# Optimization experiments

Hardware: AMD Instinct MI355X
Metric: run time of the kernel (lower is better)

## Reference

```python
import jax, jax.numpy as jnp
import numpy as np


def _knn_graph(x, k):
    """Faithful port of DynamicLstmGnn.knn_to_graph + get_u_v, returning the
    dense symmetrized edge-weight matrix [N, N] (the original re-sparsifies
    this same matrix via coalesce; nonzero extraction is data-dependent and
    not jit-able, so the dense matrix is the canonical output)."""
    N = x.shape[0]
    # negative squared euclidean distance: -||xi||^2 + 2 xi.xj - ||xj||^2
    xx = jnp.sum(x * x, axis=1, keepdims=True)          # [N, 1]
    inner = -2.0 * (x @ x.T)                              # [N, N]
    pairwise_distance = -xx - inner - xx.T                # [N, N], <= 0
    vals, idx = jax.lax.top_k(pairwise_distance, k)       # [N, k] largest (= closest)
    rows = jnp.repeat(jnp.arange(N), k)                   # idx_prime.flatten()
    # sparse COO -> to_dense (duplicate indices sum, matching torch.sparse)
    edges = jnp.zeros((N, N), dtype=x.dtype).at[rows, idx.ravel()].add(vals.ravel())
    edges_int = (edges > 0).astype(x.dtype)
    reflected_int = edges_int + edges_int.T
    reflected_edges = edges + edges.T
    denom = jnp.where(reflected_int == 0, jnp.ones((), x.dtype), reflected_int)
    edges = reflected_edges / denom
    diag = jnp.arange(N)
    edges = edges.at[diag, diag].set(0.0)                 # fill_diagonal_(0)
    return edges


def setup_inputs() -> dict:
    key = jax.random.key(0)
    x = jax.random.normal(key, (10000, 64), dtype=jnp.float32)
    return {"x": x, "k": 5}


def reference(x, k):
    return _knn_graph(x, k)
```

## Files before the change

### kernel.cpp

```cpp
#include <hip/hip_runtime.h>
#include <math.h>
#include <limits.h>

#define D 64
#define K 5
#define LK 8
#define GK 12
#define NSPLIT 16
#define NTILES 625
#define ROWBLK 157
#define NCOMP (ROWBLK * NSPLIT)
typedef unsigned int u32;
typedef unsigned long long u64;
typedef __bf16 bf16x8 __attribute__((ext_vector_type(8)));
typedef float  f32x4v __attribute__((ext_vector_type(4)));

__device__ __forceinline__ u32 med3u(u32 a, u32 b, u32 c) {
    u32 r;
    asm("v_med3_u32 %0, %1, %2, %3" : "=v"(r) : "v"(a), "v"(b), "v"(c));
    return r;
}

__device__ __forceinline__ u32 pack32(float v, int idx) {
    u32 u = __float_as_uint(v);
    u ^= ((u32)((int)u >> 31)) | 0x80000000u;
    return (u & 0xFFFFC000u) | ((~(u32)idx) & 0x3FFFu);
}
__device__ __forceinline__ int idx32(u32 key) { return (int)((~key) & 0x3FFFu); }

__device__ __forceinline__ u64 packKV(float v, int idx) {
    u32 u = __float_as_uint(v);
    u ^= ((u32)((int)u >> 31)) | 0x80000000u;
    return ((u64)u << 32) | (u32)(~idx);
}
__device__ __forceinline__ float unpackV(u64 key) {
    u32 hu = (u32)(key >> 32);
    return (hu & 0x80000000u) ? __uint_as_float(hu & 0x7fffffffu)
                              : __uint_as_float(~hu);
}

template<int LO, int LA, int LB, typename T>
__device__ __forceinline__ void mergeKeep(T a[LA], const T b[LB]) {
    T A[LA], B[LB], out[LO];
#pragma unroll
    for (int i = 0; i < LA; ++i) A[i] = a[i];
#pragma unroll
    for (int i = 0; i < LB; ++i) B[i] = b[i];
#pragma unroll
    for (int m = 0; m < LO; ++m) {
        bool ta = A[0] >= B[0];
        out[m] = ta ? A[0] : B[0];
#pragma unroll
        for (int i = 0; i < LA - 1; ++i) A[i] = ta ? A[i + 1] : A[i];
        A[LA - 1] = ta ? (T)0 : A[LA - 1];
#pragma unroll
        for (int i = 0; i < LB - 1; ++i) B[i] = ta ? B[i] : B[i + 1];
        B[LB - 1] = ta ? B[LB - 1] : (T)0;
    }
#pragma unroll
    for (int m = 0; m < LO; ++m) a[m] = out[m];
}

__global__ __launch_bounds__(256) void prep(
    const float* __restrict__ x, __bf16* __restrict__ xbA, float* __restrict__ xxf, int N)
{
    int g = blockIdx.x * 256 + threadIdx.x;
    const int REPACK = NTILES * 2 * 64;
    if (g < REPACK) {
        int tile = g >> 7;
        int rem  = g & 127;
        int kh   = rem >> 6;
        int lane = rem & 63;
        int q = lane >> 4, r = lane & 15;
        int row = tile * 16 + r;
        int k0  = kh * 32 + q * 8;
        const float4* p = (const float4*)(x + (size_t)row * D + k0);
        float4 v0 = p[0], v1 = p[1];
        bf16x8 o;
        o[0] = (__bf16)v0.x; o[1] = (__bf16)v0.y; o[2] = (__bf16)v0.z; o[3] = (__bf16)v0.w;
        o[4] = (__bf16)v1.x; o[5] = (__bf16)v1.y; o[6] = (__bf16)v1.z; o[7] = (__bf16)v1.w;
        ((bf16x8*)xbA)[g] = o;
        return;
    }
    int i = g - REPACK;
    if (i >= N) return;
    const float4* p = (const float4*)(x + (size_t)i * D);
    float s = 0.f;
#pragma unroll
    for (int t = 0; t < 16; ++t) {
        float4 v = p[t];
        s += v.x * v.x + v.y * v.y + v.z * v.z + v.w * v.w;
    }
    xxf[i] = s;
}

__global__ __launch_bounds__(256) void topk_zero_mfma(
    const __bf16* __restrict__ xbA, const float* __restrict__ xxf, int N,
    u32* __restrict__ wsK, float* __restrict__ outZ, long long totalF4,
    int nZero, int f4PerZ)
{
    const int bx  = blockIdx.x;
    const int tid = threadIdx.x;

    if (bx % 6 == 0) {
        int zid = bx / 6;
        if (zid >= nZero) return;
        long long s = (long long)zid * f4PerZ;
        long long e = s + f4PerZ; if (e > totalF4) e = totalF4;
        const f32x4v z = {0.f, 0.f, 0.f, 0.f};
        for (long long i = s + tid; i < e; i += 256)
            __builtin_nontemporal_store(z, (f32x4v*)(outZ + 4 * i));
        return;
    }

    const int cid = bx - (bx / 6 + 1);
    if (cid >= NCOMP) return;
    const int split = cid / ROWBLK;
    const int rb    = cid - split * ROWBLK;

    const int lane = tid & 63;
    const int wave = tid >> 6;
    const int l15  = lane & 15;
    const int q    = lane >> 4;
    const int r0 = rb * 64 + wave * 16;

    const bf16x8* fb = (const bf16x8*)xbA;

    int bt = r0 >> 4; if (bt > NTILES - 1) bt = NTILES - 1;
    const bf16x8 B0 = fb[bt * 128 + lane];
    const bf16x8 B1 = fb[bt * 128 + 64 + lane];

    const bf16x8* ap = fb + (size_t)split * 128 + lane;
    const float* xcp = xxf + split * 16 + q * 4;
    int cbase = split * 16 + q * 4;
    const int apBump = NSPLIT * 128;
    const int xcBump = NSPLIT * 16;

    u32 L[LK];
#pragma unroll
    for (int m = 0; m < LK; ++m) L[m] = 0u;

    for (int t = split; t < NTILES; t += NSPLIT) {
        const bf16x8 A0 = ap[0];
        const bf16x8 A1 = ap[64];
        const f32x4v xc = *(const f32x4v*)xcp;
        ap += apBump;
        xcp += xcBump;

        f32x4v acc = {0.f, 0.f, 0.f, 0.f};
        acc = __builtin_amdgcn_mfma_f32_16x16x32_bf16(A0, B0, acc, 0, 0, 0);
        acc = __builtin_amdgcn_mfma_f32_16x16x32_bf16(A1, B1, acc, 0, 0, 0);

#pragma unroll
        for (int v = 0; v < 4; ++v) {
            float dk = fmaf(-0.5f, xc[v], acc[v]);
            u32 key = pack32(dk, cbase + v);
            u32 n0 = max(L[0], key);
            u32 n1 = med3u(L[0], L[1], key);
            u32 n2 = med3u(L[1], L[2], key);
            u32 n3 = med3u(L[2], L[3], key);
            u32 n4 = med3u(L[3], L[4], key);
            u32 n5 = med3u(L[4], L[5], key);
            u32 n6 = med3u(L[5], L[6], key);
            u32 n7 = med3u(L[6], L[7], key);
            L[0]=n0; L[1]=n1; L[2]=n2; L[3]=n3; L[4]=n4; L[5]=n5; L[6]=n6; L[7]=n7;
        }
        cbase += xcBump;
    }

#pragma unroll
    for (int mask = 16; mask <= 32; mask <<= 1) {
        u32 P[LK];
#pragma unroll
        for (int m = 0; m < LK; ++m) P[m] = (u32)__shfl_xor((int)L[m], mask);
        mergeKeep<LK, LK, LK, u32>(L, P);
    }

    if (lane < 16) {
        int row = r0 + l15;
        if (row < N) {
            u32* dst = wsK + ((size_t)row * NSPLIT + split) * LK;
#pragma unroll
            for (int m = 0; m < LK; ++m) dst[m] = L[m];
        }
    }
}

__global__ __launch_bounds__(256) void rescore_scatter(
    const u32* __restrict__ wsK, const float* __restrict__ x, const float* __restrict__ xxf,
    float* __restrict__ out, int N)
{
    const int lane = threadIdx.x & 63;
    const int wave = threadIdx.x >> 6;
    const int sub  = lane & 3;
    const int row  = blockIdx.x * 64 + wave * 16 + (lane >> 2);
    const bool vrow = (row < N);
    const int rr = vrow ? row : 0;

    u32 cur[GK];
    {
        const u32* Lp = wsK + ((size_t)rr * NSPLIT + 4 * sub) * LK;
#pragma unroll
        for (int m = 0; m < LK; ++m) cur[m] = Lp[m];
#pragma unroll
        for (int m = LK; m < GK; ++m) cur[m] = 0u;
#pragma unroll
        for (int l = 1; l < 4; ++l) {
            u32 b[LK];
#pragma unroll
            for (int m = 0; m < LK; ++m) b[m] = Lp[l * LK + m];
            mergeKeep<GK, GK, LK, u32>(cur, b);
        }
    }
#pragma unroll
    for (int mask = 1; mask <= 2; mask <<= 1) {
        u32 P[GK];
#pragma unroll
        for (int m = 0; m < GK; ++m) P[m] = (u32)__shfl_xor((int)cur[m], mask);
        mergeKeep<GK, GK, GK, u32>(cur, P);
    }

    const float nxi = xxf[rr];
    int   cj[3]; bool cval[3];
    float d[3] = {0.f, 0.f, 0.f};
    const f32x4v* pj[3];
#pragma unroll
    for (int c = 0; c < 3; ++c) {
        int j = idx32(cur[sub * 3 + c]);
        cval[c] = (j < N) && (cur[sub * 3 + c] != 0u);
        cj[c] = cval[c] ? j : 0;
        pj[c] = (const f32x4v*)(x + (size_t)cj[c] * D);
    }
    const f32x4v* xip = (const f32x4v*)(x + (size_t)rr * D);
#pragma unroll
    for (int t = 0; t < 16; ++t) {
        const f32x4v xv = xip[t];
#pragma unroll
        for (int c = 0; c < 3; ++c) {
            const f32x4v pv = pj[c][t];
            d[c] = fmaf(xv[0], pv[0], d[c]);
            d[c] = fmaf(xv[1], pv[1], d[c]);
            d[c] = fmaf(xv[2], pv[2], d[c]);
            d[c] = fmaf(xv[3], pv[3], d[c]);
        }
    }
    u64 F[K];
#pragma unroll
    for (int c = 0; c < 3; ++c) {
        float val = 2.f * d[c] - nxi - xxf[cj[c]];
        F[c] = cval[c] ? packKV(val, cj[c]) : 0ull;
    }
    F[3] = 0ull; F[4] = 0ull;
    { u64 a0=F[0],a1=F[1],a2=F[2];
      if (a0 < a1) { u64 t0=a0; a0=a1; a1=t0; }
      if (a1 < a2) { u64 t0=a1; a1=a2; a2=t0; }
      if (a0 < a1) { u64 t0=a0; a0=a1; a1=t0; }
      F[0]=a0; F[1]=a1; F[2]=a2; }
#pragma unroll
    for (int mask = 1; mask <= 2; mask <<= 1) {
        u64 P[K];
#pragma unroll
        for (int m = 0; m < K; ++m) P[m] = __shfl_xor(F[m], mask);
        mergeKeep<K, K, K, u64>(F, P);
    }

    if (sub == 0 && vrow) {
#pragma unroll
        for (int m = 0; m < K; ++m) {
            int j = (int)(~(u32)F[m]);
            if ((unsigned)j < (unsigned)N && j != row) {
                float v = unpackV(F[m]);
                atomicAdd(out + (size_t)row * N + j, v);
                atomicAdd(out + (size_t)j * N + row, v);
            }
        }
    }
}

extern "C" void kernel_launch(void* const* d_in, const int* in_sizes, int n_in,
                              void* d_out, int out_size, void* d_ws, size_t ws_size,
                              hipStream_t stream) {
    const float* x = (const float*)d_in[0];
    const int N = in_sizes[0] / D;
    float* out = (float*)d_out;

    const size_t oXB = 0;
    const size_t oXX = ((size_t)NTILES * 2 * 64 * 8 * 2 + 255) & ~255ull;
    const size_t oWK = (oXX + (size_t)N * 4 + 255) & ~255ull;
    __bf16* xbA = (__bf16*)((char*)d_ws + oXB);
    float*  xxf = (float*)((char*)d_ws + oXX);
    u32*    wsK = (u32*)((char*)d_ws + oWK);

    const int prepThreads = NTILES * 2 * 64 + N;
    prep<<<(prepThreads + 255) / 256, 256, 0, stream>>>(x, xbA, xxf, N);

    long long totalF4 = (long long)out_size / 4;
    const int nBlocksTotal = 3024;
    const int nZero = (nBlocksTotal + 5) / 6;
    int f4PerZ = (int)((totalF4 + nZero - 1) / nZero);
    topk_zero_mfma<<<nBlocksTotal, 256, 0, stream>>>(
        xbA, xxf, N, wsK, out, totalF4, nZero, f4PerZ);

    rescore_scatter<<<ROWBLK, 256, 0, stream>>>(wsK, x, xxf, out, N);
}
```

Baseline: 450.7 us.

## Fuse top-k selection and rescoring into one per-tile kernel, move zeroing to prep

Merges the split top-k MFMA kernel and the rescore/scatter kernel into one kernel. Each block owns one 16-row tile, and its four waves stride over the column tiles. Partial candidate lists are merged through shared memory instead of a global workspace, and the loop prefetches the next A tile and norms. Output zeroing moves into the prep kernel, which removes one launch and the workspace round trip. In exchange, zeroing no longer overlaps the distance computation, each wave's serial selection chain is four times longer, and far fewer waves are in flight to hide latency.

```diff
diff --git a/kernel.cpp b/kernel.cpp
--- a/kernel.cpp
+++ b/kernel.cpp
@@ -1,15 +1,12 @@
 #include <hip/hip_runtime.h>
-#include <math.h>
-#include <limits.h>
 
 #define D 64
 #define K 5
 #define LK 8
 #define GK 12
-#define NSPLIT 16
 #define NTILES 625
-#define ROWBLK 157
-#define NCOMP (ROWBLK * NSPLIT)
+#define PREPBLK 352
+#define NZBLK 4096
 typedef unsigned int u32;
 typedef unsigned long long u64;
 typedef __bf16 bf16x8 __attribute__((ext_vector_type(8)));
@@ -61,91 +58,85 @@
     for (int m = 0; m < LO; ++m) a[m] = out[m];
 }
 
-__global__ __launch_bounds__(256) void prep(
-    const float* __restrict__ x, __bf16* __restrict__ xbA, float* __restrict__ xxf, int N)
+__global__ __launch_bounds__(256) void prep_zero(
+    const float* __restrict__ x, __bf16* __restrict__ xbA, float* __restrict__ xxf,
+    int N, float* __restrict__ outZ, long long totalF4, int f4PerZ)
 {
-    int g = blockIdx.x * 256 + threadIdx.x;
-    const int REPACK = NTILES * 2 * 64;
-    if (g < REPACK) {
-        int tile = g >> 7;
-        int rem  = g & 127;
-        int kh   = rem >> 6;
-        int lane = rem & 63;
-        int q = lane >> 4, r = lane & 15;
-        int row = tile * 16 + r;
-        int k0  = kh * 32 + q * 8;
-        const float4* p = (const float4*)(x + (size_t)row * D + k0);
-        float4 v0 = p[0], v1 = p[1];
-        bf16x8 o;
-        o[0] = (__bf16)v0.x; o[1] = (__bf16)v0.y; o[2] = (__bf16)v0.z; o[3] = (__bf16)v0.w;
-        o[4] = (__bf16)v1.x; o[5] = (__bf16)v1.y; o[6] = (__bf16)v1.z; o[7] = (__bf16)v1.w;
-        ((bf16x8*)xbA)[g] = o;
+    const int bx = blockIdx.x;
+    const int tid = threadIdx.x;
+
+    if (bx < PREPBLK) {
+        int g = bx * 256 + tid;
+        const int REPACK = NTILES * 2 * 64;
+        if (g < REPACK) {
+            int tile = g >> 7;
+            int rem  = g & 127;
+            int kh   = rem >> 6;
+            int lane = rem & 63;
+            int q = lane >> 4, r = lane & 15;
+            int row = tile * 16 + r;
+            int k0  = kh * 32 + q * 8;
+            const float4* p = (const float4*)(x + (size_t)row * D + k0);
+            float4 v0 = p[0], v1 = p[1];
+            bf16x8 o;
+            o[0] = (__bf16)v0.x; o[1] = (__bf16)v0.y; o[2] = (__bf16)v0.z; o[3] = (__bf16)v0.w;
+            o[4] = (__bf16)v1.x; o[5] = (__bf16)v1.y; o[6] = (__bf16)v1.z; o[7] = (__bf16)v1.w;
+            ((bf16x8*)xbA)[g] = o;
+            return;
+        }
+        int i = g - REPACK;
+        if (i >= N) return;
+        const float4* p = (const float4*)(x + (size_t)i * D);
+        float s = 0.f;
+#pragma unroll
+        for (int t = 0; t < 16; ++t) {
+            float4 v = p[t];
+            s += v.x * v.x + v.y * v.y + v.z * v.z + v.w * v.w;
+        }
+        xxf[i] = s;
         return;
     }
-    int i = g - REPACK;
-    if (i >= N) return;
-    const float4* p = (const float4*)(x + (size_t)i * D);
-    float s = 0.f;
-#pragma unroll
-    for (int t = 0; t < 16; ++t) {
-        float4 v = p[t];
-        s += v.x * v.x + v.y * v.y + v.z * v.z + v.w * v.w;
-    }
-    xxf[i] = s;
-}
-
-__global__ __launch_bounds__(256) void topk_zero_mfma(
-    const __bf16* __restrict__ xbA, const float* __restrict__ xxf, int N,
-    u32* __restrict__ wsK, float* __restrict__ outZ, long long totalF4,
-    int nZero, int f4PerZ)
+
+    int zid = bx - PREPBLK;
+    long long s = (long long)zid * f4PerZ;
+    long long e = s + f4PerZ; if (e > totalF4) e = totalF4;
+    const f32x4v z = {0.f, 0.f, 0.f, 0.f};
+    for (long long i = s + tid; i < e; i += 256)
+        __builtin_nontemporal_store(z, (f32x4v*)(outZ + 4 * i));
+}
+
+__global__ __launch_bounds__(256) void knn_select(
+    const __bf16* __restrict__ xbA, const float* __restrict__ xxf,
+    const float* __restrict__ x, int N, float* __restrict__ out)
 {
-    const int bx  = blockIdx.x;
-    const int tid = threadIdx.x;
-
-    if (bx % 6 == 0) {
-        int zid = bx / 6;
-        if (zid >= nZero) return;
-        long long s = (long long)zid * f4PerZ;
-        long long e = s + f4PerZ; if (e > totalF4) e = totalF4;
-        const f32x4v z = {0.f, 0.f, 0.f, 0.f};
-        for (long long i = s + tid; i < e; i += 256)
-            __builtin_nontemporal_store(z, (f32x4v*)(outZ + 4 * i));
-        return;
-    }
-
-    const int cid = bx - (bx / 6 + 1);
-    if (cid >= NCOMP) return;
-    const int split = cid / ROWBLK;
-    const int rb    = cid - split * ROWBLK;
-
+    const int rb   = blockIdx.x;
+    const int tid  = threadIdx.x;
     const int lane = tid & 63;
     const int wave = tid >> 6;
-    const int l15  = lane & 15;
     const int q    = lane >> 4;
-    const int r0 = rb * 64 + wave * 16;
 
     const bf16x8* fb = (const bf16x8*)xbA;
-
-    int bt = r0 >> 4; if (bt > NTILES - 1) bt = NTILES - 1;
-    const bf16x8 B0 = fb[bt * 128 + lane];
-    const bf16x8 B1 = fb[bt * 128 + 64 + lane];
-
-    const bf16x8* ap = fb + (size_t)split * 128 + lane;
-    const float* xcp = xxf + split * 16 + q * 4;
-    int cbase = split * 16 + q * 4;
-    const int apBump = NSPLIT * 128;
-    const int xcBump = NSPLIT * 16;
+    const bf16x8 B0 = fb[rb * 128 + lane];
+    const bf16x8 B1 = fb[rb * 128 + 64 + lane];
+
+    const int t0 = wave ^ 3;
+    const bf16x8* ap = fb + (size_t)t0 * 128 + lane;
+    const float*  xcp = xxf + t0 * 16 + q * 4;
+    int cbase = t0 * 16 + q * 4;
 
     u32 L[LK];
 #pragma unroll
     for (int m = 0; m < LK; ++m) L[m] = 0u;
 
-    for (int t = split; t < NTILES; t += NSPLIT) {
-        const bf16x8 A0 = ap[0];
-        const bf16x8 A1 = ap[64];
-        const f32x4v xc = *(const f32x4v*)xcp;
-        ap += apBump;
-        xcp += xcBump;
+    bf16x8 A0 = ap[0];
+    bf16x8 A1 = ap[64];
+    f32x4v xc = *(const f32x4v*)xcp;
+
+    for (int t = t0; t < NTILES; t += 4) {
+        ap += 512; xcp += 64;
+        const bf16x8 nA0 = ap[0];
+        const bf16x8 nA1 = ap[64];
+        const f32x4v nxc = *(const f32x4v*)xcp;
 
         f32x4v acc = {0.f, 0.f, 0.f, 0.f};
         acc = __builtin_amdgcn_mfma_f32_16x16x32_bf16(A0, B0, acc, 0, 0, 0);
@@ -165,7 +156,8 @@
             u32 n7 = med3u(L[6], L[7], key);
             L[0]=n0; L[1]=n1; L[2]=n2; L[3]=n3; L[4]=n4; L[5]=n5; L[6]=n6; L[7]=n7;
         }
-        cbase += xcBump;
+        cbase += 64;
+        A0 = nA0; A1 = nA1; xc = nxc;
     }
 
 #pragma unroll
@@ -176,42 +168,25 @@
         mergeKeep<LK, LK, LK, u32>(L, P);
     }
 
+    __shared__ u32 lsd[4][16][LK];
     if (lane < 16) {
-        int row = r0 + l15;
-        if (row < N) {
-            u32* dst = wsK + ((size_t)row * NSPLIT + split) * LK;
-#pragma unroll
-            for (int m = 0; m < LK; ++m) dst[m] = L[m];
-        }
-    }
-}
-
-__global__ __launch_bounds__(256) void rescore_scatter(
-    const u32* __restrict__ wsK, const float* __restrict__ x, const float* __restrict__ xxf,
-    float* __restrict__ out, int N)
-{
-    const int lane = threadIdx.x & 63;
-    const int wave = threadIdx.x >> 6;
-    const int sub  = lane & 3;
-    const int row  = blockIdx.x * 64 + wave * 16 + (lane >> 2);
+#pragma unroll
+        for (int m = 0; m < LK; ++m) lsd[wave][lane][m] = L[m];
+    }
+    __syncthreads();
+    if (wave != 0) return;
+
+    const int sub = lane & 3;
+    const int rl  = lane >> 2;
+    const int row = rb * 16 + rl;
     const bool vrow = (row < N);
     const int rr = vrow ? row : 0;
 
     u32 cur[GK];
-    {
-        const u32* Lp = wsK + ((size_t)rr * NSPLIT + 4 * sub) * LK;
-#pragma unroll
-        for (int m = 0; m < LK; ++m) cur[m] = Lp[m];
-#pragma unroll
-        for (int m = LK; m < GK; ++m) cur[m] = 0u;
-#pragma unroll
-        for (int l = 1; l < 4; ++l) {
-            u32 b[LK];
-#pragma unroll
-            for (int m = 0; m < LK; ++m) b[m] = Lp[l * LK + m];
-            mergeKeep<GK, GK, LK, u32>(cur, b);
-        }
-    }
+#pragma unroll
+    for (int m = 0; m < LK; ++m) cur[m] = lsd[sub][rl][m];
+#pragma unroll
+    for (int m = LK; m < GK; ++m) cur[m] = 0u;
 #pragma unroll
     for (int mask = 1; mask <= 2; mask <<= 1) {
         u32 P[GK];
@@ -252,9 +227,9 @@
     }
     F[3] = 0ull; F[4] = 0ull;
     { u64 a0=F[0],a1=F[1],a2=F[2];
-      if (a0 < a1) { u64 t0=a0; a0=a1; a1=t0; }
-      if (a1 < a2) { u64 t0=a1; a1=a2; a2=t0; }
-      if (a0 < a1) { u64 t0=a0; a0=a1; a1=t0; }
+      if (a0 < a1) { u64 t0s=a0; a0=a1; a1=t0s; }
+      if (a1 < a2) { u64 t0s=a1; a1=a2; a2=t0s; }
+      if (a0 < a1) { u64 t0s=a0; a0=a1; a1=t0s; }
       F[0]=a0; F[1]=a1; F[2]=a2; }
 #pragma unroll
     for (int mask = 1; mask <= 2; mask <<= 1) {
@@ -285,21 +260,13 @@
     float* out = (float*)d_out;
 
     const size_t oXB = 0;
-    const size_t oXX = ((size_t)NTILES * 2 * 64 * 8 * 2 + 255) & ~255ull;
-    const size_t oWK = (oXX + (size_t)N * 4 + 255) & ~255ull;
+    const size_t oXX = 0x150000;
     __bf16* xbA = (__bf16*)((char*)d_ws + oXB);
     float*  xxf = (float*)((char*)d_ws + oXX);
-    u32*    wsK = (u32*)((char*)d_ws + oWK);
-
-    const int prepThreads = NTILES * 2 * 64 + N;
-    prep<<<(prepThreads + 255) / 256, 256, 0, stream>>>(x, xbA, xxf, N);
 
     long long totalF4 = (long long)out_size / 4;
-    const int nBlocksTotal = 3024;
-    const int nZero = (nBlocksTotal + 5) / 6;
-    int f4PerZ = (int)((totalF4 + nZero - 1) / nZero);
-    topk_zero_mfma<<<nBlocksTotal, 256, 0, stream>>>(
-        xbA, xxf, N, wsK, out, totalF4, nZero, f4PerZ);
-
-    rescore_scatter<<<ROWBLK, 256, 0, stream>>>(wsK, x, xxf, out, N);
-}
+    int f4PerZ = (int)((totalF4 + NZBLK - 1) / NZBLK);
+
+    prep_zero<<<PREPBLK + NZBLK, 256, 0, stream>>>(x, xbA, xxf, N, out, totalF4, f4PerZ);
+    knn_select<<<NTILES, 256, 0, stream>>>(xbA, xxf, x, N, out);
+}
```

Measured after the change: 568.4 us. 26.1% more time.
